# Kernel tuning notes

Hardware: AMD Instinct MI355X
Metric: run time of the kernel (lower is better)

The kernel has to match this reference:

```python
import jax, jax.numpy as jnp
import numpy as np

D_MODEL = 4096
HIDDEN = int(8 * D_MODEL / 3)  # 10922, as in the torch __init__
QMAX = 127.0

def fake_quant(t):
    """Symmetric per-tensor int8 fake-quantization (quantize -> dequantize).
    Emulates the quantize/dequantize boundaries of nn.quantized.Linear."""
    s = jnp.maximum(jnp.max(jnp.abs(t)) / QMAX, 1e-8)
    return jnp.clip(jnp.round(t / s), -QMAX, QMAX) * s

def setup_inputs() -> dict:
    key = jax.random.key(0)
    kx, kg, ku, kd, kbg, kbu, kbd = jax.random.split(key, 7)
    x = jax.random.normal(kx, (4096, D_MODEL), dtype=jnp.float32)
    # int8 weights stored dequantized in fp32 (scale * int8 grid applied in fake_quant)
    std = 1.0 / np.sqrt(D_MODEL)
    wg = jax.random.normal(kg, (HIDDEN, D_MODEL), dtype=jnp.float32) * std
    wu = jax.random.normal(ku, (HIDDEN, D_MODEL), dtype=jnp.float32) * std
    wd = jax.random.normal(kd, (D_MODEL, HIDDEN), dtype=jnp.float32) * (1.0 / np.sqrt(HIDDEN))
    bg = jax.random.normal(kbg, (HIDDEN,), dtype=jnp.float32) * 0.01
    bu = jax.random.normal(kbu, (HIDDEN,), dtype=jnp.float32) * 0.01
    bd = jax.random.normal(kbd, (D_MODEL,), dtype=jnp.float32) * 0.01
    return {"x": x, "wg": wg, "wu": wu, "wd": wd, "bg": bg, "bu": bu, "bd": bd}

def reference(x, wg, wu, wd, bg, bu, bd):
    # int8 quantized SwiGLU expert: each nn.quantized.Linear quantizes its
    # input, uses int8 weights, and emits a (re)quantized output.
    xq = fake_quant(x)
    gate = fake_quant(jnp.einsum('td,hd->th', xq, fake_quant(wg)) + bg)
    up = fake_quant(jnp.einsum('td,hd->th', xq, fake_quant(wu)) + bu)
    act = fake_quant(jax.nn.silu(gate) * up)  # SwiGLU, requantized at down_proj input
    out = jnp.einsum('th,dh->td', act, fake_quant(wd)) + bd
    return out
```

## Files before the change

kernel.cpp:

```cpp
#include <hip/hip_runtime.h>

#define D_MODEL 4096
#define HID     10922
#define HIDP    11008
#define MTOK    4096
#define QMAXF   127.0f

typedef _Float16 half8  __attribute__((ext_vector_type(8)));
typedef _Float16 half4v __attribute__((ext_vector_type(4)));
typedef float    floatx4 __attribute__((ext_vector_type(4)));

__device__ __forceinline__ void gl_lds16(const void* g, void* l) {
  __builtin_amdgcn_global_load_lds((__attribute__((address_space(1))) void*)g,
                                   (__attribute__((address_space(3))) void*)l,
                                   16, 0, 0);
}

__device__ __forceinline__ float slot_scale(const unsigned* slots, int idx) {
  return fmaxf(__uint_as_float(slots[idx]) / QMAXF, 1e-8f);
}

__global__ void absmax_k(const float* __restrict__ in, int n4, unsigned* __restrict__ slot) {
  int tid = blockIdx.x * blockDim.x + threadIdx.x;
  int stride = gridDim.x * blockDim.x;
  float m = 0.f;
  const float4* in4 = (const float4*)in;
  for (int i = tid; i < n4; i += stride) {
    float4 v = in4[i];
    m = fmaxf(m, fmaxf(fmaxf(fabsf(v.x), fabsf(v.y)), fmaxf(fabsf(v.z), fabsf(v.w))));
  }
  #pragma unroll
  for (int off = 32; off; off >>= 1) m = fmaxf(m, __shfl_down(m, off));
  __shared__ float sm[4];
  int lane = threadIdx.x & 63, w = threadIdx.x >> 6;
  if (!lane) sm[w] = m;
  __syncthreads();
  if (!threadIdx.x) {
    m = fmaxf(fmaxf(sm[0], sm[1]), fmaxf(sm[2], sm[3]));
    atomicMax(slot, __float_as_uint(m));
  }
}

__global__ void quant_k(const float* __restrict__ in, _Float16* __restrict__ out,
                        int rows_in, int cols_in, int cols_out, int total8,
                        const unsigned* __restrict__ slot) {
  float s = fmaxf(__uint_as_float(*slot) / QMAXF, 1e-8f);
  int t = blockIdx.x * blockDim.x + threadIdx.x;
  if (t >= total8) return;
  int idx = t * 8;
  int r = idx / cols_out;
  int c = idx - r * cols_out;
  half8 h;
  if (r < rows_in && c + 8 <= cols_in) {
    const float2* p = (const float2*)(in + (size_t)r * cols_in + c);
    #pragma unroll
    for (int j = 0; j < 4; ++j) {
      float2 v = p[j];
      float q0 = fminf(fmaxf(rintf(v.x / s), -QMAXF), QMAXF);
      float q1 = fminf(fmaxf(rintf(v.y / s), -QMAXF), QMAXF);
      h[2 * j]     = (_Float16)q0;
      h[2 * j + 1] = (_Float16)q1;
    }
  } else {
    #pragma unroll
    for (int j = 0; j < 8; ++j) {
      int cc = c + j;
      float v = 0.f;
      if (r < rows_in && cc < cols_in) v = in[(size_t)r * cols_in + cc];
      float q = fminf(fmaxf(rintf(v / s), -QMAXF), QMAXF);
      h[j] = (_Float16)q;
    }
  }
  *(half8*)(out + idx) = h;
}

__device__ __forceinline__ float act_val(float g, float u, float sg, float su) {
  float gq = fminf(fmaxf(rintf(g / sg), -QMAXF), QMAXF) * sg;
  float uq = fminf(fmaxf(rintf(u / su), -QMAXF), QMAXF) * su;
  float sig = (gq >= 0.f) ? (1.f / (1.f + expf(-gq)))
                          : (expf(gq) / (1.f + expf(gq)));
  return (gq * sig) * uq;
}

__global__ void act_max_k(const float* __restrict__ gate, const float* __restrict__ up,
                          const unsigned* __restrict__ slots, unsigned* __restrict__ outslot,
                          int n4) {
  float sg = slot_scale(slots, 4);
  float su = slot_scale(slots, 5);
  int tid = blockIdx.x * blockDim.x + threadIdx.x;
  int stride = gridDim.x * blockDim.x;
  float m = 0.f;
  const float4* g4 = (const float4*)gate;
  const float4* u4 = (const float4*)up;
  for (int i = tid; i < n4; i += stride) {
    float4 g = g4[i], u = u4[i];
    m = fmaxf(m, fabsf(act_val(g.x, u.x, sg, su)));
    m = fmaxf(m, fabsf(act_val(g.y, u.y, sg, su)));
    m = fmaxf(m, fabsf(act_val(g.z, u.z, sg, su)));
    m = fmaxf(m, fabsf(act_val(g.w, u.w, sg, su)));
  }
  #pragma unroll
  for (int off = 32; off; off >>= 1) m = fmaxf(m, __shfl_down(m, off));
  __shared__ float sm[4];
  int lane = threadIdx.x & 63, w = threadIdx.x >> 6;
  if (!lane) sm[w] = m;
  __syncthreads();
  if (!threadIdx.x) {
    m = fmaxf(fmaxf(sm[0], sm[1]), fmaxf(sm[2], sm[3]));
    atomicMax(outslot, __float_as_uint(m));
  }
}

__global__ void act_quant_k(const float* __restrict__ gate, const float* __restrict__ up,
                            const unsigned* __restrict__ slots, _Float16* __restrict__ actq,
                            int n4) {
  float sg = slot_scale(slots, 4);
  float su = slot_scale(slots, 5);
  float sa = slot_scale(slots, 6);
  int tid = blockIdx.x * blockDim.x + threadIdx.x;
  int stride = gridDim.x * blockDim.x;
  const float4* g4 = (const float4*)gate;
  const float4* u4 = (const float4*)up;
  for (int i = tid; i < n4; i += stride) {
    float4 g = g4[i], u = u4[i];
    float a0 = act_val(g.x, u.x, sg, su);
    float a1 = act_val(g.y, u.y, sg, su);
    float a2 = act_val(g.z, u.z, sg, su);
    float a3 = act_val(g.w, u.w, sg, su);
    half4v h;
    h[0] = (_Float16)fminf(fmaxf(rintf(a0 / sa), -QMAXF), QMAXF);
    h[1] = (_Float16)fminf(fmaxf(rintf(a1 / sa), -QMAXF), QMAXF);
    h[2] = (_Float16)fminf(fmaxf(rintf(a2 / sa), -QMAXF), QMAXF);
    h[3] = (_Float16)fminf(fmaxf(rintf(a3 / sa), -QMAXF), QMAXF);
    *(half4v*)(actq + (size_t)i * 4) = h;
  }
}


#define SBAR() do {                                                           \
    __builtin_amdgcn_sched_barrier(0);                                        \
    __builtin_amdgcn_s_barrier();                                             \
    __builtin_amdgcn_sched_barrier(0);                                        \
  } while (0)

#define STAGE(GB, LS, LD, TB, KT, BUF, H) do {                                \
    const char* _s = (GB) + ((size_t)((TB) + (H) * 128 + s_r0) * (LD)         \
                             + (size_t)(KT) * 64) * 2 + s_cb;                 \
    char* _d = (char*)(LS) + ((BUF) * 2 + (H)) * 16384 + wave * 1024;         \
    gl_lds16(_s, _d);                                                         \
    gl_lds16(_s + (size_t)(LD) * 128, _d + 8192);                             \
  } while (0)

#define PHASE(BUF, HM, HN, ...) do {                                          \
    half8 af[4][2], bf[2][2];                                                 \
    _Pragma("unroll")                                                         \
    for (int i2 = 0; i2 < 4; ++i2) {                                          \
      int gr = (HM) * 128 + wrow * 64 + i2 * 16 + l16;                        \
      const char* pa = (const char*)As + ((BUF) * 2 + (gr >> 7)) * 16384      \
                       + (gr & 127) * 128;                                    \
      _Pragma("unroll")                                                       \
      for (int ks = 0; ks < 2; ++ks)                                          \
        af[i2][ks] = *(const half8*)(pa + (((ks * 4 + quad) ^ (l16 & 7)) * 16)); \
    }                                                                         \
    _Pragma("unroll")                                                         \
    for (int j2 = 0; j2 < 2; ++j2) {                                          \
      int gc = (HN) * 128 + wcol * 32 + j2 * 16 + l16;                        \
      const char* pb = (const char*)Bs + ((BUF) * 2 + (gc >> 7)) * 16384      \
                       + (gc & 127) * 128;                                    \
      _Pragma("unroll")                                                       \
      for (int ks = 0; ks < 2; ++ks)                                          \
        bf[j2][ks] = *(const half8*)(pb + (((ks * 4 + quad) ^ (l16 & 7)) * 16)); \
    }                                                                         \
    __VA_ARGS__;                                                              \
    SBAR();                                                                   \
    __builtin_amdgcn_s_setprio(1);                                            \
    _Pragma("unroll")                                                         \
    for (int i2 = 0; i2 < 4; ++i2)                                            \
      _Pragma("unroll")                                                       \
      for (int j2 = 0; j2 < 2; ++j2)                                          \
        _Pragma("unroll")                                                     \
        for (int ks = 0; ks < 2; ++ks)                                        \
          acc[(HM) * 4 + i2][(HN) * 2 + j2] =                                 \
              __builtin_amdgcn_mfma_f32_16x16x32_f16(                         \
                  af[i2][ks], bf[j2][ks],                                     \
                  acc[(HM) * 4 + i2][(HN) * 2 + j2], 0, 0, 0);                \
    __builtin_amdgcn_s_setprio(0);                                            \
    SBAR();                                                                   \
  } while (0)

__global__ __launch_bounds__(512, 2) void gemm_k(
    const _Float16* __restrict__ A, const _Float16* __restrict__ B,
    const float* __restrict__ bias, float* __restrict__ C,
    int K, int lda, int ldb, int ldc, int nbias,
    const unsigned* __restrict__ slots, int sa_idx, int sb_idx,
    unsigned* __restrict__ maxslot) {
  __shared__ __align__(16) _Float16 As[2 * 2 * 128 * 64];
  __shared__ __align__(16) _Float16 Bs[2 * 2 * 128 * 64];
  __shared__ float smx[8];

  const int tid = threadIdx.x;
  const int wave = tid >> 6, lane = tid & 63;
  const int wrow = wave >> 2, wcol = wave & 3;
  const int l16 = lane & 15, quad = lane >> 4;
  const int tm = blockIdx.x * 256, tn = blockIdx.y * 256;

  const int s_r0 = wave * 8 + (lane >> 3);
  const int s_cb = ((lane & 7) ^ (lane >> 3)) * 16;

  const char* Ab = (const char*)A;
  const char* Bb = (const char*)B;

  floatx4 acc[8][4] = {};

  const int NT = K >> 6;

  STAGE(Ab, As, lda, tm, 0, 0, 0);
  STAGE(Ab, As, lda, tm, 0, 0, 1);
  STAGE(Bb, Bs, ldb, tn, 0, 0, 0);
  STAGE(Bb, Bs, ldb, tn, 0, 0, 1);
  STAGE(Ab, As, lda, tm, 1, 1, 0);
  STAGE(Bb, Bs, ldb, tn, 1, 1, 0);
  asm volatile("s_waitcnt vmcnt(4)" ::: "memory");
  SBAR();

  for (int kt = 0; kt + 2 < NT; kt += 2) {
    PHASE(0, 0, 0, STAGE(Ab, As, lda, tm, kt + 1, 1, 1));
    PHASE(0, 0, 1, STAGE(Bb, Bs, ldb, tn, kt + 1, 1, 1));
    PHASE(0, 1, 0, STAGE(Ab, As, lda, tm, kt + 2, 0, 0));
    PHASE(0, 1, 1, {
      STAGE(Bb, Bs, ldb, tn, kt + 2, 0, 0);
      asm volatile("s_waitcnt vmcnt(4)" ::: "memory");
    });
    PHASE(1, 0, 0, STAGE(Ab, As, lda, tm, kt + 2, 0, 1));
    PHASE(1, 0, 1, STAGE(Bb, Bs, ldb, tn, kt + 2, 0, 1));
    PHASE(1, 1, 0, STAGE(Ab, As, lda, tm, kt + 3, 1, 0));
    PHASE(1, 1, 1, {
      STAGE(Bb, Bs, ldb, tn, kt + 3, 1, 0);
      asm volatile("s_waitcnt vmcnt(4)" ::: "memory");
    });
  }

  {
    const int kt = NT - 2;
    PHASE(0, 0, 0, STAGE(Ab, As, lda, tm, kt + 1, 1, 1));
    PHASE(0, 0, 1, STAGE(Bb, Bs, ldb, tn, kt + 1, 1, 1));
    PHASE(0, 1, 0, );
    PHASE(0, 1, 1, asm volatile("s_waitcnt vmcnt(0)" ::: "memory"));
    PHASE(1, 0, 0, );
    PHASE(1, 0, 1, );
    PHASE(1, 1, 0, );
    PHASE(1, 1, 1, );
  }
  asm volatile("s_waitcnt vmcnt(0)" ::: "memory");

  float scale = slot_scale(slots, sa_idx) * slot_scale(slots, sb_idx);
  float mloc = 0.f;
  #pragma unroll
  for (int i = 0; i < 8; ++i) {
    int rg0 = tm + (i >> 2) * 128 + wrow * 64 + (i & 3) * 16 + quad * 4;
    #pragma unroll
    for (int j = 0; j < 4; ++j) {
      int cg = tn + (j >> 1) * 128 + wcol * 32 + (j & 1) * 16 + l16;
      float bv = (cg < nbias) ? bias[cg] : 0.f;
      #pragma unroll
      for (int r = 0; r < 4; ++r) {
        float v = acc[i][j][r] * scale + bv;
        C[(size_t)(rg0 + r) * ldc + cg] = v;
        mloc = fmaxf(mloc, fabsf(v));
      }
    }
  }
  #pragma unroll
  for (int off = 32; off; off >>= 1) mloc = fmaxf(mloc, __shfl_down(mloc, off));
  if (!lane) smx[wave] = mloc;
  __syncthreads();
  if (!tid) {
    float m = smx[0];
    #pragma unroll
    for (int w = 1; w < 8; ++w) m = fmaxf(m, smx[w]);
    atomicMax(maxslot, __float_as_uint(m));
  }
}

extern "C" void kernel_launch(void* const* d_in, const int* in_sizes, int n_in,
                              void* d_out, int out_size, void* d_ws, size_t ws_size,
                              hipStream_t stream) {
  const float* x  = (const float*)d_in[0];
  const float* wg = (const float*)d_in[1];
  const float* wu = (const float*)d_in[2];
  const float* wd = (const float*)d_in[3];
  const float* bg = (const float*)d_in[4];
  const float* bu = (const float*)d_in[5];
  const float* bd = (const float*)d_in[6];
  float* out = (float*)d_out;

  char* ws = (char*)d_ws;
  unsigned* slots = (unsigned*)ws;
  const size_t XQ_B = (size_t)MTOK * D_MODEL * 2;
  const size_t WQ_B = (size_t)HIDP * D_MODEL * 2;
  const size_t GU_B = (size_t)MTOK * HIDP * 4;

  _Float16* xq   = (_Float16*)(ws + 256);
  _Float16* wgq  = (_Float16*)(ws + 256 + XQ_B);
  _Float16* wuq  = (_Float16*)(ws + 256 + XQ_B + WQ_B);
  float*    gate = (float*)   (ws + 256 + XQ_B + 2 * WQ_B);
  float*    up   = (float*)   (ws + 256 + XQ_B + 2 * WQ_B + GU_B);
  _Float16* actq = wgq;
  _Float16* wdq  = wuq;

  hipMemsetAsync(ws, 0, 256, stream);

  absmax_k<<<2048, 256, 0, stream>>>(x,  MTOK * D_MODEL / 4, slots + 0);
  absmax_k<<<2048, 256, 0, stream>>>(wg, HID * D_MODEL / 4,  slots + 1);
  absmax_k<<<2048, 256, 0, stream>>>(wu, HID * D_MODEL / 4,  slots + 2);
  absmax_k<<<2048, 256, 0, stream>>>(wd, MTOK * HID / 4,     slots + 3);

  {
    int t8 = MTOK * D_MODEL / 8;
    quant_k<<<(t8 + 255) / 256, 256, 0, stream>>>(x, xq, MTOK, D_MODEL, D_MODEL, t8, slots + 0);
    int w8 = HIDP * D_MODEL / 8;
    quant_k<<<(w8 + 255) / 256, 256, 0, stream>>>(wg, wgq, HID, D_MODEL, D_MODEL, w8, slots + 1);
    quant_k<<<(w8 + 255) / 256, 256, 0, stream>>>(wu, wuq, HID, D_MODEL, D_MODEL, w8, slots + 2);
  }

  {
    dim3 g1(MTOK / 256, HIDP / 256);
    gemm_k<<<g1, 512, 0, stream>>>(xq, wgq, bg, gate, D_MODEL, D_MODEL, D_MODEL, HIDP, HID,
                                   slots, 0, 1, slots + 4);
    gemm_k<<<g1, 512, 0, stream>>>(xq, wuq, bu, up,   D_MODEL, D_MODEL, D_MODEL, HIDP, HID,
                                   slots, 0, 2, slots + 5);
  }

  {
    int t8 = MTOK * HIDP / 8;
    quant_k<<<(t8 + 255) / 256, 256, 0, stream>>>(wd, wdq, MTOK, HID, HIDP, t8, slots + 3);
  }

  {
    int n4 = MTOK * HIDP / 4;
    act_max_k<<<4096, 256, 0, stream>>>(gate, up, slots, slots + 6, n4);
    act_quant_k<<<4096, 256, 0, stream>>>(gate, up, slots, actq, n4);
  }

  {
    dim3 g2(MTOK / 256, D_MODEL / 256);
    gemm_k<<<g2, 512, 0, stream>>>(actq, wdq, bd, out, HIDP, HIDP, HIDP, D_MODEL, D_MODEL,
                                   slots, 6, 3, slots + 7);
  }
}
```

Before: 2.161 ms.

## Remap workgroups for L2 locality and defer vmcnt waits past MFMAs

Workgroup IDs are remapped with an XCD-style swizzle (stride-8 interleave), so tiles that share A or B rows tend to run near each other in time. The intent is better L2/MALL reuse on the multi-die GPU. The global-load vmcnt wait now sits after each phase's MFMA block instead of before it, and some sched_barriers around the pre-MFMA s_barrier are dropped. Loads therefore get more time to overlap with compute. The tile decode assumes a 16-tile M dimension and a workgroup count divisible by 8, and removing the scheduling fences lets the compiler reorder LDS reads around the barrier.

```diff
diff --git a/kernel.cpp b/kernel.cpp
--- a/kernel.cpp
+++ b/kernel.cpp
@@ -137,11 +137,9 @@
 }
 
 
-#define SBAR() do {                                                           \
-    __builtin_amdgcn_sched_barrier(0);                                        \
-    __builtin_amdgcn_s_barrier();                                             \
-    __builtin_amdgcn_sched_barrier(0);                                        \
-  } while (0)
+#define NOOP ((void)0)
+#define VM4() asm volatile("s_waitcnt vmcnt(4)" ::: "memory")
+#define VM0() asm volatile("s_waitcnt vmcnt(0)" ::: "memory")
 
 #define STAGE(GB, LS, LD, TB, KT, BUF, H) do {                                \
     const char* _s = (GB) + ((size_t)((TB) + (H) * 128 + s_r0) * (LD)         \
@@ -151,7 +149,7 @@
     gl_lds16(_s + (size_t)(LD) * 128, _d + 8192);                             \
   } while (0)
 
-#define PHASE(BUF, HM, HN, ...) do {                                          \
+#define PHASE(BUF, HM, HN, STG, WT) do {                                      \
     half8 af[4][2], bf[2][2];                                                 \
     _Pragma("unroll")                                                         \
     for (int i2 = 0; i2 < 4; ++i2) {                                          \
@@ -171,8 +169,8 @@
       for (int ks = 0; ks < 2; ++ks)                                          \
         bf[j2][ks] = *(const half8*)(pb + (((ks * 4 + quad) ^ (l16 & 7)) * 16)); \
     }                                                                         \
-    __VA_ARGS__;                                                              \
-    SBAR();                                                                   \
+    STG;                                                                      \
+    __builtin_amdgcn_s_barrier();                                             \
     __builtin_amdgcn_s_setprio(1);                                            \
     _Pragma("unroll")                                                         \
     for (int i2 = 0; i2 < 4; ++i2)                                            \
@@ -185,7 +183,9 @@
                   af[i2][ks], bf[j2][ks],                                     \
                   acc[(HM) * 4 + i2][(HN) * 2 + j2], 0, 0, 0);                \
     __builtin_amdgcn_s_setprio(0);                                            \
-    SBAR();                                                                   \
+    WT;                                                                       \
+    __builtin_amdgcn_s_barrier();                                             \
+    __builtin_amdgcn_sched_barrier(0);                                        \
   } while (0)
 
 __global__ __launch_bounds__(512, 2) void gemm_k(
@@ -202,7 +202,12 @@
   const int wave = tid >> 6, lane = tid & 63;
   const int wrow = wave >> 2, wcol = wave & 3;
   const int l16 = lane & 15, quad = lane >> 4;
-  const int tm = blockIdx.x * 256, tn = blockIdx.y * 256;
+
+  const int nwg  = gridDim.x * gridDim.y;
+  const int flat = blockIdx.y * gridDim.x + blockIdx.x;
+  const int swz  = (flat & 7) * (nwg >> 3) + (flat >> 3);
+  const int tm = (swz & 15) * 256;
+  const int tn = (swz >> 4) * 256;
 
   const int s_r0 = wave * 8 + (lane >> 3);
   const int s_cb = ((lane & 7) ^ (lane >> 3)) * 16;
@@ -220,38 +225,33 @@
   STAGE(Bb, Bs, ldb, tn, 0, 0, 1);
   STAGE(Ab, As, lda, tm, 1, 1, 0);
   STAGE(Bb, Bs, ldb, tn, 1, 1, 0);
-  asm volatile("s_waitcnt vmcnt(4)" ::: "memory");
-  SBAR();
+  VM4();
+  __builtin_amdgcn_s_barrier();
+  __builtin_amdgcn_sched_barrier(0);
 
   for (int kt = 0; kt + 2 < NT; kt += 2) {
-    PHASE(0, 0, 0, STAGE(Ab, As, lda, tm, kt + 1, 1, 1));
-    PHASE(0, 0, 1, STAGE(Bb, Bs, ldb, tn, kt + 1, 1, 1));
-    PHASE(0, 1, 0, STAGE(Ab, As, lda, tm, kt + 2, 0, 0));
-    PHASE(0, 1, 1, {
-      STAGE(Bb, Bs, ldb, tn, kt + 2, 0, 0);
-      asm volatile("s_waitcnt vmcnt(4)" ::: "memory");
-    });
-    PHASE(1, 0, 0, STAGE(Ab, As, lda, tm, kt + 2, 0, 1));
-    PHASE(1, 0, 1, STAGE(Bb, Bs, ldb, tn, kt + 2, 0, 1));
-    PHASE(1, 1, 0, STAGE(Ab, As, lda, tm, kt + 3, 1, 0));
-    PHASE(1, 1, 1, {
-      STAGE(Bb, Bs, ldb, tn, kt + 3, 1, 0);
-      asm volatile("s_waitcnt vmcnt(4)" ::: "memory");
-    });
+    PHASE(0, 0, 0, STAGE(Ab, As, lda, tm, kt + 1, 1, 1), NOOP);
+    PHASE(0, 0, 1, STAGE(Bb, Bs, ldb, tn, kt + 1, 1, 1), NOOP);
+    PHASE(0, 1, 0, STAGE(Ab, As, lda, tm, kt + 2, 0, 0), NOOP);
+    PHASE(0, 1, 1, STAGE(Bb, Bs, ldb, tn, kt + 2, 0, 0), VM4());
+    PHASE(1, 0, 0, STAGE(Ab, As, lda, tm, kt + 2, 0, 1), NOOP);
+    PHASE(1, 0, 1, STAGE(Bb, Bs, ldb, tn, kt + 2, 0, 1), NOOP);
+    PHASE(1, 1, 0, STAGE(Ab, As, lda, tm, kt + 3, 1, 0), NOOP);
+    PHASE(1, 1, 1, STAGE(Bb, Bs, ldb, tn, kt + 3, 1, 0), VM4());
   }
 
   {
     const int kt = NT - 2;
-    PHASE(0, 0, 0, STAGE(Ab, As, lda, tm, kt + 1, 1, 1));
-    PHASE(0, 0, 1, STAGE(Bb, Bs, ldb, tn, kt + 1, 1, 1));
-    PHASE(0, 1, 0, );
-    PHASE(0, 1, 1, asm volatile("s_waitcnt vmcnt(0)" ::: "memory"));
-    PHASE(1, 0, 0, );
-    PHASE(1, 0, 1, );
-    PHASE(1, 1, 0, );
-    PHASE(1, 1, 1, );
-  }
-  asm volatile("s_waitcnt vmcnt(0)" ::: "memory");
+    PHASE(0, 0, 0, STAGE(Ab, As, lda, tm, kt + 1, 1, 1), NOOP);
+    PHASE(0, 0, 1, STAGE(Bb, Bs, ldb, tn, kt + 1, 1, 1), NOOP);
+    PHASE(0, 1, 0, NOOP, NOOP);
+    PHASE(0, 1, 1, NOOP, VM0());
+    PHASE(1, 0, 0, NOOP, NOOP);
+    PHASE(1, 0, 1, NOOP, NOOP);
+    PHASE(1, 1, 0, NOOP, NOOP);
+    PHASE(1, 1, 1, NOOP, NOOP);
+  }
+  VM0();
 
   float scale = slot_scale(slots, sa_idx) * slot_scale(slots, sb_idx);
   float mloc = 0.f;
```

New measurement: 2.162 ms. Within noise of the previous version (+0.0%).

## Restructure GEMM main loop into four half-M phases with B fragments held in registers

Applied to the files above, without the earlier changes.

The GEMM inner loop moves from eight quarter-tile phases per two K-tiles to four half-M phases. The full B fragment set (4x2 half8) is loaded once per K-tile and kept in registers across both M halves, which removes redundant LDS reads of B and halves the number of barriers per tile. The global-to-LDS staging order and vmcnt waits are rescheduled to fit the new phases (vmcnt 2 instead of 4). Each phase now issues 32 MFMAs. The cost is more register pressure, and the new staging order puts the correctness of the LDS buffer reuse at risk.

```diff
diff --git a/kernel.cpp b/kernel.cpp
--- a/kernel.cpp
+++ b/kernel.cpp
@@ -137,11 +137,10 @@
 }
 
 
-#define SBAR() do {                                                           \
-    __builtin_amdgcn_sched_barrier(0);                                        \
-    __builtin_amdgcn_s_barrier();                                             \
-    __builtin_amdgcn_sched_barrier(0);                                        \
-  } while (0)
+#define VM2() asm volatile("s_waitcnt vmcnt(2)" ::: "memory")
+#define VM0() asm volatile("s_waitcnt vmcnt(0)" ::: "memory")
+#define BAR() __builtin_amdgcn_s_barrier()
+#define SCHED0() __builtin_amdgcn_sched_barrier(0)
 
 #define STAGE(GB, LS, LD, TB, KT, BUF, H) do {                                \
     const char* _s = (GB) + ((size_t)((TB) + (H) * 128 + s_r0) * (LD)         \
@@ -151,8 +150,19 @@
     gl_lds16(_s + (size_t)(LD) * 128, _d + 8192);                             \
   } while (0)
 
-#define PHASE(BUF, HM, HN, ...) do {                                          \
-    half8 af[4][2], bf[2][2];                                                 \
+#define LOAD_BF(BUF) do {                                                     \
+    _Pragma("unroll")                                                         \
+    for (int j2 = 0; j2 < 4; ++j2) {                                          \
+      int gc = (j2 >> 1) * 128 + wcol * 32 + (j2 & 1) * 16 + l16;             \
+      const char* pb = (const char*)Bs + ((BUF) * 2 + (gc >> 7)) * 16384      \
+                       + (gc & 127) * 128;                                    \
+      _Pragma("unroll")                                                       \
+      for (int ks = 0; ks < 2; ++ks)                                          \
+        bf[j2][ks] = *(const half8*)(pb + (((ks * 4 + quad) ^ (l16 & 7)) * 16)); \
+    }                                                                         \
+  } while (0)
+
+#define LOAD_AF(BUF, HM) do {                                                 \
     _Pragma("unroll")                                                         \
     for (int i2 = 0; i2 < 4; ++i2) {                                          \
       int gr = (HM) * 128 + wrow * 64 + i2 * 16 + l16;                        \
@@ -162,30 +172,19 @@
       for (int ks = 0; ks < 2; ++ks)                                          \
         af[i2][ks] = *(const half8*)(pa + (((ks * 4 + quad) ^ (l16 & 7)) * 16)); \
     }                                                                         \
-    _Pragma("unroll")                                                         \
-    for (int j2 = 0; j2 < 2; ++j2) {                                          \
-      int gc = (HN) * 128 + wcol * 32 + j2 * 16 + l16;                        \
-      const char* pb = (const char*)Bs + ((BUF) * 2 + (gc >> 7)) * 16384      \
-                       + (gc & 127) * 128;                                    \
-      _Pragma("unroll")                                                       \
-      for (int ks = 0; ks < 2; ++ks)                                          \
-        bf[j2][ks] = *(const half8*)(pb + (((ks * 4 + quad) ^ (l16 & 7)) * 16)); \
-    }                                                                         \
-    __VA_ARGS__;                                                              \
-    SBAR();                                                                   \
+  } while (0)
+
+#define MFMA32(HM) do {                                                       \
     __builtin_amdgcn_s_setprio(1);                                            \
     _Pragma("unroll")                                                         \
     for (int i2 = 0; i2 < 4; ++i2)                                            \
       _Pragma("unroll")                                                       \
-      for (int j2 = 0; j2 < 2; ++j2)                                          \
+      for (int j2 = 0; j2 < 4; ++j2)                                          \
         _Pragma("unroll")                                                     \
         for (int ks = 0; ks < 2; ++ks)                                        \
-          acc[(HM) * 4 + i2][(HN) * 2 + j2] =                                 \
-              __builtin_amdgcn_mfma_f32_16x16x32_f16(                         \
-                  af[i2][ks], bf[j2][ks],                                     \
-                  acc[(HM) * 4 + i2][(HN) * 2 + j2], 0, 0, 0);                \
+          acc[(HM) * 4 + i2][j2] = __builtin_amdgcn_mfma_f32_16x16x32_f16(    \
+              af[i2][ks], bf[j2][ks], acc[(HM) * 4 + i2][j2], 0, 0, 0);       \
     __builtin_amdgcn_s_setprio(0);                                            \
-    SBAR();                                                                   \
   } while (0)
 
 __global__ __launch_bounds__(512, 2) void gemm_k(
@@ -211,47 +210,100 @@
   const char* Bb = (const char*)B;
 
   floatx4 acc[8][4] = {};
+  half8 bf[4][2];
 
   const int NT = K >> 6;
 
   STAGE(Ab, As, lda, tm, 0, 0, 0);
-  STAGE(Ab, As, lda, tm, 0, 0, 1);
   STAGE(Bb, Bs, ldb, tn, 0, 0, 0);
   STAGE(Bb, Bs, ldb, tn, 0, 0, 1);
+  STAGE(Ab, As, lda, tm, 0, 0, 1);
   STAGE(Ab, As, lda, tm, 1, 1, 0);
-  STAGE(Bb, Bs, ldb, tn, 1, 1, 0);
-  asm volatile("s_waitcnt vmcnt(4)" ::: "memory");
-  SBAR();
+  VM2();
+  BAR();
+  SCHED0();
 
   for (int kt = 0; kt + 2 < NT; kt += 2) {
-    PHASE(0, 0, 0, STAGE(Ab, As, lda, tm, kt + 1, 1, 1));
-    PHASE(0, 0, 1, STAGE(Bb, Bs, ldb, tn, kt + 1, 1, 1));
-    PHASE(0, 1, 0, STAGE(Ab, As, lda, tm, kt + 2, 0, 0));
-    PHASE(0, 1, 1, {
+    {
+      half8 af[4][2];
+      LOAD_BF(0);
+      LOAD_AF(0, 0);
+      STAGE(Ab, As, lda, tm, kt + 1, 1, 1);
+      STAGE(Bb, Bs, ldb, tn, kt + 1, 1, 0);
+      STAGE(Bb, Bs, ldb, tn, kt + 1, 1, 1);
+      BAR();
+      MFMA32(0);
+      BAR(); SCHED0();
+    }
+    {
+      half8 af[4][2];
+      LOAD_AF(0, 1);
+      STAGE(Ab, As, lda, tm, kt + 2, 0, 0);
+      BAR();
+      MFMA32(1);
+      VM2();
+      BAR(); SCHED0();
+    }
+    {
+      half8 af[4][2];
+      LOAD_BF(1);
+      LOAD_AF(1, 0);
+      STAGE(Ab, As, lda, tm, kt + 2, 0, 1);
       STAGE(Bb, Bs, ldb, tn, kt + 2, 0, 0);
-      asm volatile("s_waitcnt vmcnt(4)" ::: "memory");
-    });
-    PHASE(1, 0, 0, STAGE(Ab, As, lda, tm, kt + 2, 0, 1));
-    PHASE(1, 0, 1, STAGE(Bb, Bs, ldb, tn, kt + 2, 0, 1));
-    PHASE(1, 1, 0, STAGE(Ab, As, lda, tm, kt + 3, 1, 0));
-    PHASE(1, 1, 1, {
-      STAGE(Bb, Bs, ldb, tn, kt + 3, 1, 0);
-      asm volatile("s_waitcnt vmcnt(4)" ::: "memory");
-    });
+      STAGE(Bb, Bs, ldb, tn, kt + 2, 0, 1);
+      BAR();
+      MFMA32(0);
+      BAR(); SCHED0();
+    }
+    {
+      half8 af[4][2];
+      LOAD_AF(1, 1);
+      STAGE(Ab, As, lda, tm, kt + 3, 1, 0);
+      BAR();
+      MFMA32(1);
+      VM2();
+      BAR(); SCHED0();
+    }
   }
 
   {
     const int kt = NT - 2;
-    PHASE(0, 0, 0, STAGE(Ab, As, lda, tm, kt + 1, 1, 1));
-    PHASE(0, 0, 1, STAGE(Bb, Bs, ldb, tn, kt + 1, 1, 1));
-    PHASE(0, 1, 0, );
-    PHASE(0, 1, 1, asm volatile("s_waitcnt vmcnt(0)" ::: "memory"));
-    PHASE(1, 0, 0, );
-    PHASE(1, 0, 1, );
-    PHASE(1, 1, 0, );
-    PHASE(1, 1, 1, );
-  }
-  asm volatile("s_waitcnt vmcnt(0)" ::: "memory");
+    {
+      half8 af[4][2];
+      LOAD_BF(0);
+      LOAD_AF(0, 0);
+      STAGE(Ab, As, lda, tm, kt + 1, 1, 1);
+      STAGE(Bb, Bs, ldb, tn, kt + 1, 1, 0);
+      STAGE(Bb, Bs, ldb, tn, kt + 1, 1, 1);
+      BAR();
+      MFMA32(0);
+      BAR(); SCHED0();
+    }
+    {
+      half8 af[4][2];
+      LOAD_AF(0, 1);
+      BAR();
+      MFMA32(1);
+      VM0();
+      BAR(); SCHED0();
+    }
+    {
+      half8 af[4][2];
+      LOAD_BF(1);
+      LOAD_AF(1, 0);
+      BAR();
+      MFMA32(0);
+      BAR(); SCHED0();
+    }
+    {
+      half8 af[4][2];
+      LOAD_AF(1, 1);
+      BAR();
+      MFMA32(1);
+      BAR(); SCHED0();
+    }
+  }
+  VM0();
 
   float scale = slot_scale(slots, sa_idx) * slot_scale(slots, sb_idx);
   float mloc = 0.f;
```

Measured after the change: 2.039 ms. -5.6%, faster.
